# Kernel tuning notes

Measured on AMD Instinct MI355X. Metric: run time of the kernel, lower is better.

Reference implementation:

```python
import jax, jax.numpy as jnp
import numpy as np

B, N, D, S = 128, 1024, 512, 64
ITERS = 3
EPS = 1e-8


def setup_inputs() -> dict:
    key = jax.random.key(0)
    ks = jax.random.split(key, 10)
    inp = {
        "inputs_pe": jax.random.normal(ks[0], (B, N, D), dtype=jnp.float32),
        "inputs": jax.random.normal(ks[1], (B, N, D), dtype=jnp.float32),
        "slots": jax.random.normal(ks[2], (1, S, D), dtype=jnp.float32),
        "W1": jax.random.normal(ks[3], (D, D), dtype=jnp.float32) * 0.02,
        "b1": jnp.zeros((D,), dtype=jnp.float32),
        "W2": jax.random.normal(ks[4], (D, D), dtype=jnp.float32) * 0.02,
        "b2": jnp.zeros((D,), dtype=jnp.float32),
        "W3": jax.random.normal(ks[5], (D, D), dtype=jnp.float32) * 0.02,
        "b3": jnp.zeros((D,), dtype=jnp.float32),
    }
    return inp


def reference(inputs_pe, inputs, slots, W1, b1, W2, b2, W3, b3):
    b = inputs_pe.shape[0]
    scale = D ** (-0.5)
    # to_k: Linear -> ReLU -> Linear -> ReLU -> Linear (torch Linear: x @ W.T + b)
    h = jax.nn.relu(jnp.einsum('bnd,ed->bne', inputs_pe, W1) + b1)
    h = jax.nn.relu(jnp.einsum('bnd,ed->bne', h, W2) + b2)
    k = jnp.einsum('bnd,ed->bne', h, W3) + b3  # [b, n, d]

    q = jnp.broadcast_to(slots, (b, S, D))  # slots never updated in the loop
    for _ in range(ITERS):
        dots = jnp.einsum('bid,bjd->bij', q, k) * scale  # [b, S, n]
        s_j = dots.sum(axis=2, keepdims=True)            # sum over keys j -> [b, S, 1]
        s_all = dots.sum(axis=(1, 2), keepdims=True)     # total per batch -> [b, 1, 1]
        dots = dots / s_j * s_all
        attn = jax.nn.sigmoid(dots)
        attn2 = attn / (attn.sum(axis=-1, keepdims=True) + EPS)
        updates = jnp.einsum('bjd,bij->bid', inputs, attn2)  # [b, S, d]
    return updates, attn
```

## Files before the change

kernel.cpp:

```cpp
#include <hip/hip_runtime.h>
#include <stdint.h>

#define Bb 128
#define Nn 1024
#define Dd 512
#define Ss 64

constexpr float kScale = 0.044194173824159216f;
constexpr float kEps = 1e-8f;

typedef __bf16 bf16x8 __attribute__((ext_vector_type(8)));
typedef float f32x4 __attribute__((ext_vector_type(4)));
typedef float f32x16 __attribute__((ext_vector_type(16)));

__device__ inline unsigned short f2bf_rne(float x) {
  unsigned u = __builtin_bit_cast(unsigned, x);
  u += 0x7FFFu + ((u >> 16) & 1u);
  return (unsigned short)(u >> 16);
}
__device__ inline float bf2f(unsigned short h) {
  unsigned u = ((unsigned)h) << 16;
  return __builtin_bit_cast(float, u);
}

__device__ inline void gl_lds16(const void* g, void* l) {
  typedef unsigned int u32;
  auto gp = (u32 __attribute__((address_space(1)))*)(unsigned long long)(uintptr_t)g;
  auto lp = (u32 __attribute__((address_space(3)))*)(unsigned int)(uintptr_t)l;
  __builtin_amdgcn_global_load_lds(gp, lp, 16, 0, 0);
}

__global__ void cast_split(const float* __restrict__ in,
                           unsigned short* __restrict__ hi,
                           unsigned short* __restrict__ lo,
                           int n4) {
  int i = blockIdx.x * blockDim.x + threadIdx.x;
  const int stride = gridDim.x * blockDim.x;
  for (; i < n4; i += stride) {
    const float4 v = ((const float4*)in)[i];
    ushort4 h, lw;
    h.x = f2bf_rne(v.x); lw.x = f2bf_rne(v.x - bf2f(h.x));
    h.y = f2bf_rne(v.y); lw.y = f2bf_rne(v.y - bf2f(h.y));
    h.z = f2bf_rne(v.z); lw.z = f2bf_rne(v.z - bf2f(h.z));
    h.w = f2bf_rne(v.w); lw.w = f2bf_rne(v.w - bf2f(h.w));
    ((ushort4*)hi)[i] = h;
    ((ushort4*)lo)[i] = lw;
  }
}

template <int ACT>
__global__ __launch_bounds__(512, 1) void gemm_full(
    const unsigned short* __restrict__ Ah, const unsigned short* __restrict__ Al,
    const unsigned short* __restrict__ Wh, const unsigned short* __restrict__ Wl,
    const float* __restrict__ bias,
    unsigned short* __restrict__ Ch, unsigned short* __restrict__ Cl) {
  constexpr int K = 512, BK = 16;
  constexpr int NT = K / BK;
  constexpr int BUF = 20480;
  extern __shared__ unsigned short lds[];
  const int t = threadIdx.x, l = t & 63, w = t >> 6;
  const int wr = w >> 2, wc = w & 3;
  const long rowA0 = (long)blockIdx.x * 128;

  const int p = w >> 2, q = w & 3;
  const unsigned short* srcA = (p ? Al : Ah) + (rowA0 + q * 32 + (l >> 1)) * K + (l & 1) * 8;
  const int s0 = w * 2, s1 = w * 2 + 1;
  const unsigned short* srcWh0 = Wh + (long)(s0 * 32 + (l >> 1)) * K + (l & 1) * 8;
  const unsigned short* srcWh1 = Wh + (long)(s1 * 32 + (l >> 1)) * K + (l & 1) * 8;
  const unsigned short* srcWl0 = Wl + (long)(s0 * 32 + (l >> 1)) * K + (l & 1) * 8;
  const unsigned short* srcWl1 = Wl + (long)(s1 * 32 + (l >> 1)) * K + (l & 1) * 8;
  const int dA = p * 2048 + q * 512;

#define GSTAGE(bufi, koff)                                    \
  {                                                           \
    unsigned short* bq = lds + (bufi)*BUF;                    \
    gl_lds16(srcA + (koff), bq + dA);                         \
    gl_lds16(srcWh0 + (koff), bq + 4096 + s0 * 512);          \
    gl_lds16(srcWh1 + (koff), bq + 4096 + s1 * 512);          \
    gl_lds16(srcWl0 + (koff), bq + 12288 + s0 * 512);         \
    gl_lds16(srcWl1 + (koff), bq + 12288 + s1 * 512);         \
  }

  const int fra = (l & 31) * 16 + (l >> 5) * 8;

  f32x16 acc[2][4] = {};

  GSTAGE(0, 0);
  GSTAGE(1, BK);

  for (int tt = 0; tt < NT; ++tt) {
    if (tt < NT - 1) {
      asm volatile("s_waitcnt vmcnt(5)" ::: "memory");
    } else {
      asm volatile("s_waitcnt vmcnt(0)" ::: "memory");
    }
    __builtin_amdgcn_s_barrier();
    __builtin_amdgcn_sched_barrier(0);
    if (tt < NT - 2) GSTAGE((tt + 2) % 3, (tt + 2) * BK);

    const unsigned short* bufc = lds + (tt % 3) * BUF;
    bf16x8 fah[2], fal[2], fbh[4], fbl[4];
#pragma unroll
    for (int m = 0; m < 2; m++) {
      fah[m] = *(const bf16x8*)(bufc + wr * 1024 + m * 512 + fra);
      fal[m] = *(const bf16x8*)(bufc + 2048 + wr * 1024 + m * 512 + fra);
    }
#pragma unroll
    for (int n = 0; n < 4; n++) {
      fbh[n] = *(const bf16x8*)(bufc + 4096 + wc * 2048 + n * 512 + fra);
      fbl[n] = *(const bf16x8*)(bufc + 12288 + wc * 2048 + n * 512 + fra);
    }
    __builtin_amdgcn_s_setprio(1);
#pragma unroll
    for (int m = 0; m < 2; m++)
#pragma unroll
      for (int n = 0; n < 4; n++) {
        acc[m][n] = __builtin_amdgcn_mfma_f32_32x32x16_bf16(fah[m], fbh[n], acc[m][n], 0, 0, 0);
        acc[m][n] = __builtin_amdgcn_mfma_f32_32x32x16_bf16(fal[m], fbh[n], acc[m][n], 0, 0, 0);
        acc[m][n] = __builtin_amdgcn_mfma_f32_32x32x16_bf16(fah[m], fbl[n], acc[m][n], 0, 0, 0);
      }
    __builtin_amdgcn_s_setprio(0);
    __builtin_amdgcn_sched_barrier(0);
  }
#undef GSTAGE

#pragma unroll
  for (int m = 0; m < 2; m++)
#pragma unroll
    for (int n = 0; n < 4; n++) {
      const int col = wc * 128 + n * 32 + (l & 31);
      const float bv = bias[col];
#pragma unroll
      for (int r = 0; r < 16; r++) {
        const long row = rowA0 + wr * 64 + m * 32 + (r & 3) + 8 * (r >> 2) + 4 * (l >> 5);
        float x = acc[m][n][r] + bv;
        if (ACT) x = fmaxf(x, 0.0f);
        const unsigned short h = f2bf_rne(x);
        const long idx = row * 512 + col;
        Ch[idx] = h;
        Cl[idx] = f2bf_rne(x - bf2f(h));
      }
    }
}

__global__ __launch_bounds__(256) void gemm_dots_split(
    const unsigned short* __restrict__ Qh, const unsigned short* __restrict__ Ql,
    const unsigned short* __restrict__ Kh, const unsigned short* __restrict__ Kl,
    float* __restrict__ dots) {
  constexpr int K = 512, BM = 64, BN = 128, BK = 32;
  __shared__ __align__(16) unsigned short lah[BM * BK];
  __shared__ __align__(16) unsigned short lal[BM * BK];
  __shared__ __align__(16) unsigned short lbh[BN * BK];
  __shared__ __align__(16) unsigned short lbl[BN * BK];
  const int t = threadIdx.x, l = t & 63, w = t >> 6;
  const int b = blockIdx.x >> 3, bc = blockIdx.x & 7;
  const unsigned short* kh = Kh + (long)b * Nn * Dd;
  const unsigned short* kl = Kl + (long)b * Nn * Dd;
  f32x4 acc[4][2] = {};

  for (int k0 = 0; k0 < K; k0 += BK) {
    {
      const int c = t;
      const int ga = (c >> 2) * K + k0 + (c & 3) * 8;
      const int lo = (w * 64) * 8;
      gl_lds16(Qh + ga, lah + lo);
      gl_lds16(Ql + ga, lal + lo);
    }
#pragma unroll
    for (int qq = 0; qq < 2; qq++) {
      const int c = qq * 256 + t;
      const long gb = (long)(bc * BN + (c >> 2)) * K + k0 + (c & 3) * 8;
      const int lo = (qq * 256 + w * 64) * 8;
      gl_lds16(kh + gb, lbh + lo);
      gl_lds16(kl + gb, lbl + lo);
    }
    __syncthreads();
    bf16x8 ah[4], al[4], bh[2], bl[2];
#pragma unroll
    for (int m = 0; m < 4; m++) {
      const int off = (m * 16 + (l & 15)) * BK + (l >> 4) * 8;
      ah[m] = *(const bf16x8*)(lah + off);
      al[m] = *(const bf16x8*)(lal + off);
    }
#pragma unroll
    for (int n = 0; n < 2; n++) {
      const int off = (w * 32 + n * 16 + (l & 15)) * BK + (l >> 4) * 8;
      bh[n] = *(const bf16x8*)(lbh + off);
      bl[n] = *(const bf16x8*)(lbl + off);
    }
#pragma unroll
    for (int m = 0; m < 4; m++)
#pragma unroll
      for (int n = 0; n < 2; n++) {
        acc[m][n] = __builtin_amdgcn_mfma_f32_16x16x32_bf16(ah[m], bh[n], acc[m][n], 0, 0, 0);
        acc[m][n] = __builtin_amdgcn_mfma_f32_16x16x32_bf16(al[m], bh[n], acc[m][n], 0, 0, 0);
        acc[m][n] = __builtin_amdgcn_mfma_f32_16x16x32_bf16(ah[m], bl[n], acc[m][n], 0, 0, 0);
      }
    __syncthreads();
  }
  float* dp = dots + (long)b * Ss * Nn;
#pragma unroll
  for (int m = 0; m < 4; m++) {
    const int row = m * 16 + (l >> 4) * 4;
#pragma unroll
    for (int n = 0; n < 2; n++) {
      const int col = bc * BN + w * 32 + n * 16 + (l & 15);
#pragma unroll
      for (int r = 0; r < 4; r++) dp[(long)(row + r) * Nn + col] = acc[m][n][r] * kScale;
    }
  }
}

__global__ __launch_bounds__(256) void reduce_k(
    const float* __restrict__ dots, float* __restrict__ s_j, float* __restrict__ s_all) {
  const int b = blockIdx.x;
  const int t = threadIdx.x;
  const float* dp = dots + (long)b * Ss * Nn;
  const int i = t >> 2, qq = t & 3;
  float s = 0.f;
  const float* rp = dp + i * Nn + qq * 256;
  for (int j = 0; j < 256; j++) s += rp[j];
  __shared__ float part[256];
  __shared__ float rowsum[64];
  part[t] = s;
  __syncthreads();
  if (t < 64) {
    const float v = part[t * 4] + part[t * 4 + 1] + part[t * 4 + 2] + part[t * 4 + 3];
    rowsum[t] = v;
    s_j[b * 64 + t] = v;
  }
  __syncthreads();
  if (t == 0) {
    float tot = 0.f;
    for (int k = 0; k < 64; k++) tot += rowsum[k];
    s_all[b] = tot;
  }
}

__global__ __launch_bounds__(256) void attn_k(
    const float* __restrict__ dots, const float* __restrict__ s_j,
    const float* __restrict__ s_all, float* __restrict__ attn_out,
    float* __restrict__ inv_r) {
  const int bi = blockIdx.x;
  const int b = bi >> 6;
  const int t = threadIdx.x;
  const float ratio = s_all[b] / s_j[bi];
  const float* dp = dots + (long)bi * Nn;
  float* ap = attn_out + (long)bi * Nn;
  float s = 0.f;
#pragma unroll
  for (int qq = 0; qq < 4; qq++) {
    const int j = qq * 256 + t;
    const float x = dp[j] * ratio;
    const float a = 1.f / (1.f + expf(-x));
    ap[j] = a;
    s += a;
  }
  __shared__ float red[256];
  red[t] = s;
  __syncthreads();
  for (int off = 128; off > 0; off >>= 1) {
    if (t < off) red[t] += red[t + off];
    __syncthreads();
  }
  if (t == 0) inv_r[bi] = 1.f / (red[0] + kEps);
}

__global__ __launch_bounds__(256, 1) void updates_k2(
    const float* __restrict__ attn, const float* __restrict__ inputs,
    const float* __restrict__ inv_r, float* __restrict__ out0) {
  constexpr int NT2 = 32;
  constexpr int BUF_F = 10240;
  extern __shared__ float ldsf[];
  const int t = threadIdx.x, lam = t & 63, w = t >> 6;
  const int b = blockIdx.x >> 1, dt = blockIdx.x & 1;
  const int ig = t >> 5, dg = t & 31;
  const float* inb = inputs + (size_t)b * (Nn * Dd) + dt * 256;
  const float* attsrc = attn + (size_t)b * (Ss * Nn) + (size_t)(t >> 2) * Nn + (t & 3) * 8;
  float acc[8][8] = {};
  float4 ga0, ga1, gb0, gb1;

#define UISSUE(bufi, tile, G0, G1)                                        \
  {                                                                       \
    const int j0_ = (tile)*32;                                            \
    G0 = *(const float4*)(attsrc + j0_);                                  \
    G1 = *(const float4*)(attsrc + j0_ + 4);                              \
    float* db_ = ldsf + (bufi)*BUF_F;                                     \
    _Pragma("unroll") for (int i_ = 0; i_ < 8; i_++) {                    \
      const int row_ = i_ * 4 + w;                                        \
      gl_lds16(inb + (size_t)(j0_ + row_) * Dd + lam * 4, db_ + row_ * 256); \
    }                                                                     \
  }

#define UWRITE(bufi, G0, G1)                                              \
  {                                                                       \
    float* ab_ = ldsf + (bufi)*BUF_F + 8192;                              \
    const int col_ = t >> 2;                                              \
    const int r0_ = (t & 3) * 8;                                          \
    ab_[(r0_ + 0) * 64 + col_] = G0.x;                                    \
    ab_[(r0_ + 1) * 64 + col_] = G0.y;                                    \
    ab_[(r0_ + 2) * 64 + col_] = G0.z;                                    \
    ab_[(r0_ + 3) * 64 + col_] = G0.w;                                    \
    ab_[(r0_ + 4) * 64 + col_] = G1.x;                                    \
    ab_[(r0_ + 5) * 64 + col_] = G1.y;                                    \
    ab_[(r0_ + 6) * 64 + col_] = G1.z;                                    \
    ab_[(r0_ + 7) * 64 + col_] = G1.w;                                    \
  }

#define UCOMP(bufi)                                                       \
  {                                                                       \
    const float* db_ = ldsf + (bufi)*BUF_F;                               \
    const float* ab_ = db_ + 8192;                                        \
    _Pragma("unroll 4") for (int jj = 0; jj < 32; jj++) {                 \
      float av[8], vv[8];                                                 \
      *(float4*)&av[0] = *(const float4*)(ab_ + jj * 64 + ig * 8);        \
      *(float4*)&av[4] = *(const float4*)(ab_ + jj * 64 + ig * 8 + 4);    \
      *(float4*)&vv[0] = *(const float4*)(db_ + jj * 256 + dg * 8);       \
      *(float4*)&vv[4] = *(const float4*)(db_ + jj * 256 + dg * 8 + 4);   \
      _Pragma("unroll") for (int m_ = 0; m_ < 8; m_++)                    \
          _Pragma("unroll") for (int n_ = 0; n_ < 8; n_++)                \
              acc[m_][n_] = __builtin_fmaf(av[m_], vv[n_], acc[m_][n_]);  \
    }                                                                     \
  }

  UISSUE(0, 0, ga0, ga1);
  UISSUE(1, 1, gb0, gb1);
  UWRITE(0, ga0, ga1);

  for (int tt = 0; tt < NT2; tt += 2) {
    asm volatile("s_waitcnt vmcnt(10)" ::: "memory");
    UWRITE((tt + 1) % 3, gb0, gb1);
    asm volatile("s_waitcnt lgkmcnt(0)" ::: "memory");
    __builtin_amdgcn_s_barrier();
    __builtin_amdgcn_sched_barrier(0);
    if (tt < NT2 - 2) UISSUE((tt + 2) % 3, tt + 2, ga0, ga1);
    UCOMP(tt % 3);
    if (tt + 1 < NT2 - 1) {
      asm volatile("s_waitcnt vmcnt(10)" ::: "memory");
    } else {
      asm volatile("s_waitcnt vmcnt(0)" ::: "memory");
    }
    if (tt + 1 < NT2 - 1) UWRITE((tt + 2) % 3, ga0, ga1);
    asm volatile("s_waitcnt lgkmcnt(0)" ::: "memory");
    __builtin_amdgcn_s_barrier();
    __builtin_amdgcn_sched_barrier(0);
    if (tt + 1 < NT2 - 2) UISSUE((tt + 3) % 3, tt + 3, gb0, gb1);
    UCOMP((tt + 1) % 3);
  }
#undef UISSUE
#undef UWRITE
#undef UCOMP

#pragma unroll
  for (int m = 0; m < 8; m++) {
    const int i = ig * 8 + m;
    const float ir = inv_r[b * 64 + i];
    float4 o0, o1;
    o0.x = acc[m][0] * ir; o0.y = acc[m][1] * ir; o0.z = acc[m][2] * ir; o0.w = acc[m][3] * ir;
    o1.x = acc[m][4] * ir; o1.y = acc[m][5] * ir; o1.z = acc[m][6] * ir; o1.w = acc[m][7] * ir;
    float* op = out0 + (size_t)(b * 64 + i) * Dd + dt * 256 + dg * 8;
    *(float4*)op = o0;
    *(float4*)(op + 4) = o1;
  }
}

extern "C" void kernel_launch(void* const* d_in, const int* in_sizes, int n_in,
                              void* d_out, int out_size, void* d_ws, size_t ws_size,
                              hipStream_t stream) {
  (void)in_sizes; (void)n_in; (void)out_size; (void)ws_size;
  const float* inputs_pe = (const float*)d_in[0];
  const float* inputs = (const float*)d_in[1];
  const float* slots = (const float*)d_in[2];
  const float* W1 = (const float*)d_in[3];
  const float* b1 = (const float*)d_in[4];
  const float* W2 = (const float*)d_in[5];
  const float* b2 = (const float*)d_in[6];
  const float* W3 = (const float*)d_in[7];
  const float* b3 = (const float*)d_in[8];

  char* ws = (char*)d_ws;
  size_t off = 0;
  auto alloc = [&](size_t bytes) -> void* {
    void* p = ws + off;
    off += (bytes + 255) & ~(size_t)255;
    return p;
  };
  const size_t actB = (size_t)Bb * Nn * Dd * 2;
  unsigned short* Ahi = (unsigned short*)alloc(actB);
  unsigned short* Alo = (unsigned short*)alloc(actB);
  unsigned short* Bhi = (unsigned short*)alloc(actB);
  unsigned short* Blo = (unsigned short*)alloc(actB);
  unsigned short* w1h = (unsigned short*)alloc(Dd * Dd * 2);
  unsigned short* w1l = (unsigned short*)alloc(Dd * Dd * 2);
  unsigned short* w2h = (unsigned short*)alloc(Dd * Dd * 2);
  unsigned short* w2l = (unsigned short*)alloc(Dd * Dd * 2);
  unsigned short* w3h = (unsigned short*)alloc(Dd * Dd * 2);
  unsigned short* w3l = (unsigned short*)alloc(Dd * Dd * 2);
  unsigned short* sh = (unsigned short*)alloc(Ss * Dd * 2);
  unsigned short* sl = (unsigned short*)alloc(Ss * Dd * 2);
  float* dotsb = (float*)alloc((size_t)Bb * Ss * Nn * 4);
  float* s_j = (float*)alloc(Bb * Ss * 4);
  float* s_all = (float*)alloc(Bb * 4);
  float* inv_r = (float*)alloc(Bb * Ss * 4);

  float* out_updates = (float*)d_out;
  float* out_attn = out_updates + (size_t)Bb * Ss * Dd;

  const int kLds = 3 * 40 * 1024;
  hipFuncSetAttribute(reinterpret_cast<const void*>(gemm_full<1>),
                      hipFuncAttributeMaxDynamicSharedMemorySize, kLds);
  hipFuncSetAttribute(reinterpret_cast<const void*>(gemm_full<0>),
                      hipFuncAttributeMaxDynamicSharedMemorySize, kLds);
  hipFuncSetAttribute(reinterpret_cast<const void*>(updates_k2),
                      hipFuncAttributeMaxDynamicSharedMemorySize, kLds);

  cast_split<<<4096, 256, 0, stream>>>(inputs_pe, Ahi, Alo, Bb * Nn * Dd / 4);
  cast_split<<<256, 256, 0, stream>>>(W1, w1h, w1l, Dd * Dd / 4);
  cast_split<<<256, 256, 0, stream>>>(W2, w2h, w2l, Dd * Dd / 4);
  cast_split<<<256, 256, 0, stream>>>(W3, w3h, w3l, Dd * Dd / 4);
  cast_split<<<32, 256, 0, stream>>>(slots, sh, sl, Ss * Dd / 4);

  gemm_full<1><<<1024, 512, kLds, stream>>>(Ahi, Alo, w1h, w1l, b1, Bhi, Blo);
  gemm_full<1><<<1024, 512, kLds, stream>>>(Bhi, Blo, w2h, w2l, b2, Ahi, Alo);
  gemm_full<0><<<1024, 512, kLds, stream>>>(Ahi, Alo, w3h, w3l, b3, Bhi, Blo);

  gemm_dots_split<<<Bb * 8, 256, 0, stream>>>(sh, sl, Bhi, Blo, dotsb);
  reduce_k<<<Bb, 256, 0, stream>>>(dotsb, s_j, s_all);
  attn_k<<<Bb * Ss, 256, 0, stream>>>(dotsb, s_j, s_all, out_attn, inv_r);
  updates_k2<<<Bb * 2, 256, kLds, stream>>>(out_attn, inputs, inv_r, out_updates);
}
```

Measured before the change: 1.166 ms.

## Rewrite MLP GEMMs with 256x256 tiles and hi/lo split K-stream

The three MLP GEMMs now use 256x256 output tiles per block instead of 128x512. The three bf16 split products (hh, lh, hl) are handled as one K-stream of 48 steps: segment 0 is Ah·Wh, 1 is Al·Wh, 2 is Ah·Wl. The kernel also switches to 16x16x32 MFMA with a 4-stage LDS ring, XOR-swizzled LDS layout, and an XCD-aware block remap. The aim is better operand reuse per loaded byte and fewer LDS bank conflicts, in exchange for more accumulator registers and a deeper pipeline that needs 128KB of LDS.

After: 1.321 ms. 13.3% more time.

```diff
diff --git a/kernel.cpp b/kernel.cpp
--- a/kernel.cpp
+++ b/kernel.cpp
@@ -11,7 +11,6 @@
 
 typedef __bf16 bf16x8 __attribute__((ext_vector_type(8)));
 typedef float f32x4 __attribute__((ext_vector_type(4)));
-typedef float f32x16 __attribute__((ext_vector_type(16)));
 
 __device__ inline unsigned short f2bf_rne(float x) {
   unsigned u = __builtin_bit_cast(unsigned, x);
@@ -49,98 +48,98 @@
 }
 
 template <int ACT>
-__global__ __launch_bounds__(512, 1) void gemm_full(
+__global__ __launch_bounds__(512, 1) void gemm_split3(
     const unsigned short* __restrict__ Ah, const unsigned short* __restrict__ Al,
     const unsigned short* __restrict__ Wh, const unsigned short* __restrict__ Wl,
     const float* __restrict__ bias,
     unsigned short* __restrict__ Ch, unsigned short* __restrict__ Cl) {
-  constexpr int K = 512, BK = 16;
-  constexpr int NT = K / BK;
-  constexpr int BUF = 20480;
+  constexpr int NT3 = 48;
   extern __shared__ unsigned short lds[];
   const int t = threadIdx.x, l = t & 63, w = t >> 6;
+  const int x = l & 15;
   const int wr = w >> 2, wc = w & 3;
-  const long rowA0 = (long)blockIdx.x * 128;
-
-  const int p = w >> 2, q = w & 3;
-  const unsigned short* srcA = (p ? Al : Ah) + (rowA0 + q * 32 + (l >> 1)) * K + (l & 1) * 8;
-  const int s0 = w * 2, s1 = w * 2 + 1;
-  const unsigned short* srcWh0 = Wh + (long)(s0 * 32 + (l >> 1)) * K + (l & 1) * 8;
-  const unsigned short* srcWh1 = Wh + (long)(s1 * 32 + (l >> 1)) * K + (l & 1) * 8;
-  const unsigned short* srcWl0 = Wl + (long)(s0 * 32 + (l >> 1)) * K + (l & 1) * 8;
-  const unsigned short* srcWl1 = Wl + (long)(s1 * 32 + (l >> 1)) * K + (l & 1) * 8;
-  const int dA = p * 2048 + q * 512;
-
-#define GSTAGE(bufi, koff)                                    \
-  {                                                           \
-    unsigned short* bq = lds + (bufi)*BUF;                    \
-    gl_lds16(srcA + (koff), bq + dA);                         \
-    gl_lds16(srcWh0 + (koff), bq + 4096 + s0 * 512);          \
-    gl_lds16(srcWh1 + (koff), bq + 4096 + s1 * 512);          \
-    gl_lds16(srcWl0 + (koff), bq + 12288 + s0 * 512);         \
-    gl_lds16(srcWl1 + (koff), bq + 12288 + s1 * 512);         \
-  }
-
-  const int fra = (l & 31) * 16 + (l >> 5) * 8;
-
-  f32x16 acc[2][4] = {};
-
-  GSTAGE(0, 0);
-  GSTAGE(1, BK);
-
-  for (int tt = 0; tt < NT; ++tt) {
-    if (tt < NT - 1) {
-      asm volatile("s_waitcnt vmcnt(5)" ::: "memory");
+
+  const int wg = (blockIdx.x & 7) * 128 + (blockIdx.x >> 3);
+  const long rowA0 = (long)(wg >> 1) * 256;
+  const int colB0 = (wg & 1) * 256;
+  const unsigned short* Ahb = Ah + rowA0 * 512;
+  const unsigned short* Alb = Al + rowA0 * 512;
+  const unsigned short* Whb = Wh + (long)colB0 * 512;
+  const unsigned short* Wlb = Wl + (long)colB0 * 512;
+
+  const int g0 = (t & 3) ^ (((t >> 2) >> 1) & 3);
+  const int offT0 = (t >> 2) * 512 + g0 * 8;
+  const int offT1 = offT0 + 65536;
+  const int wdst = w * 512;
+
+  auto stage = [&](int kt) {
+    const int seg = kt >> 4;
+    const int k0 = (kt & 15) * 32;
+    const unsigned short* As = (seg == 1) ? Alb : Ahb;
+    const unsigned short* Bs = (seg == 2) ? Wlb : Whb;
+    unsigned short* lb = lds + (kt & 3) * 16384;
+    gl_lds16(As + offT0 + k0, lb + wdst);
+    gl_lds16(As + offT1 + k0, lb + 4096 + wdst);
+    gl_lds16(Bs + offT0 + k0, lb + 8192 + wdst);
+    gl_lds16(Bs + offT1 + k0, lb + 12288 + wdst);
+  };
+
+  const int p16 = ((l >> 4) ^ ((x >> 1) & 3)) * 16;
+  const int abase = (wr * 128 + x) * 64 + p16;
+  const int bbase = 16384 + (wc * 64 + x) * 64 + p16;
+
+  f32x4 acc[8][4] = {};
+
+  stage(0);
+  stage(1);
+  stage(2);
+
+  for (int kt = 0; kt < NT3; ++kt) {
+    if (kt < NT3 - 2) {
+      asm volatile("s_waitcnt vmcnt(8)" ::: "memory");
+    } else if (kt == NT3 - 2) {
+      asm volatile("s_waitcnt vmcnt(4)" ::: "memory");
     } else {
       asm volatile("s_waitcnt vmcnt(0)" ::: "memory");
     }
     __builtin_amdgcn_s_barrier();
     __builtin_amdgcn_sched_barrier(0);
-    if (tt < NT - 2) GSTAGE((tt + 2) % 3, (tt + 2) * BK);
-
-    const unsigned short* bufc = lds + (tt % 3) * BUF;
-    bf16x8 fah[2], fal[2], fbh[4], fbl[4];
-#pragma unroll
-    for (int m = 0; m < 2; m++) {
-      fah[m] = *(const bf16x8*)(bufc + wr * 1024 + m * 512 + fra);
-      fal[m] = *(const bf16x8*)(bufc + 2048 + wr * 1024 + m * 512 + fra);
-    }
-#pragma unroll
-    for (int n = 0; n < 4; n++) {
-      fbh[n] = *(const bf16x8*)(bufc + 4096 + wc * 2048 + n * 512 + fra);
-      fbl[n] = *(const bf16x8*)(bufc + 12288 + wc * 2048 + n * 512 + fra);
-    }
+    if (kt + 3 < NT3) stage(kt + 3);
+
+    const char* bb = (const char*)lds + (kt & 3) * 32768;
+    bf16x8 fb[4], fa[8];
+#pragma unroll
+    for (int n = 0; n < 4; n++) fb[n] = *(const bf16x8*)(bb + bbase + n * 1024);
+#pragma unroll
+    for (int m = 0; m < 8; m++) fa[m] = *(const bf16x8*)(bb + abase + m * 1024);
     __builtin_amdgcn_s_setprio(1);
 #pragma unroll
-    for (int m = 0; m < 2; m++)
-#pragma unroll
-      for (int n = 0; n < 4; n++) {
-        acc[m][n] = __builtin_amdgcn_mfma_f32_32x32x16_bf16(fah[m], fbh[n], acc[m][n], 0, 0, 0);
-        acc[m][n] = __builtin_amdgcn_mfma_f32_32x32x16_bf16(fal[m], fbh[n], acc[m][n], 0, 0, 0);
-        acc[m][n] = __builtin_amdgcn_mfma_f32_32x32x16_bf16(fah[m], fbl[n], acc[m][n], 0, 0, 0);
-      }
+    for (int m = 0; m < 8; m++)
+#pragma unroll
+      for (int n = 0; n < 4; n++)
+        acc[m][n] = __builtin_amdgcn_mfma_f32_16x16x32_bf16(fa[m], fb[n], acc[m][n], 0, 0, 0);
     __builtin_amdgcn_s_setprio(0);
     __builtin_amdgcn_sched_barrier(0);
   }
-#undef GSTAGE
-
-#pragma unroll
-  for (int m = 0; m < 2; m++)
-#pragma unroll
-    for (int n = 0; n < 4; n++) {
-      const int col = wc * 128 + n * 32 + (l & 31);
-      const float bv = bias[col];
-#pragma unroll
-      for (int r = 0; r < 16; r++) {
-        const long row = rowA0 + wr * 64 + m * 32 + (r & 3) + 8 * (r >> 2) + 4 * (l >> 5);
-        float x = acc[m][n][r] + bv;
-        if (ACT) x = fmaxf(x, 0.0f);
-        const unsigned short h = f2bf_rne(x);
-        const long idx = row * 512 + col;
+
+#pragma unroll
+  for (int n = 0; n < 4; n++) {
+    const int col = colB0 + wc * 64 + n * 16 + x;
+    const float bv = bias[col];
+#pragma unroll
+    for (int m = 0; m < 8; m++) {
+      const long row = rowA0 + wr * 128 + m * 16 + (l >> 4) * 4;
+#pragma unroll
+      for (int r = 0; r < 4; r++) {
+        float xv = acc[m][n][r] + bv;
+        if (ACT) xv = fmaxf(xv, 0.0f);
+        const unsigned short h = f2bf_rne(xv);
+        const long idx = (row + r) * 512 + col;
         Ch[idx] = h;
-        Cl[idx] = f2bf_rne(x - bf2f(h));
+        Cl[idx] = f2bf_rne(xv - bf2f(h));
       }
     }
+  }
 }
 
 __global__ __launch_bounds__(256) void gemm_dots_split(
@@ -406,13 +405,14 @@
   float* out_updates = (float*)d_out;
   float* out_attn = out_updates + (size_t)Bb * Ss * Dd;
 
-  const int kLds = 3 * 40 * 1024;
-  hipFuncSetAttribute(reinterpret_cast<const void*>(gemm_full<1>),
-                      hipFuncAttributeMaxDynamicSharedMemorySize, kLds);
-  hipFuncSetAttribute(reinterpret_cast<const void*>(gemm_full<0>),
-                      hipFuncAttributeMaxDynamicSharedMemorySize, kLds);
+  const int kLdsG = 4 * 32 * 1024;
+  const int kLdsU = 3 * 40 * 1024;
+  hipFuncSetAttribute(reinterpret_cast<const void*>(gemm_split3<1>),
+                      hipFuncAttributeMaxDynamicSharedMemorySize, kLdsG);
+  hipFuncSetAttribute(reinterpret_cast<const void*>(gemm_split3<0>),
+                      hipFuncAttributeMaxDynamicSharedMemorySize, kLdsG);
   hipFuncSetAttribute(reinterpret_cast<const void*>(updates_k2),
-                      hipFuncAttributeMaxDynamicSharedMemorySize, kLds);
+                      hipFuncAttributeMaxDynamicSharedMemorySize, kLdsU);
 
   cast_split<<<4096, 256, 0, stream>>>(inputs_pe, Ahi, Alo, Bb * Nn * Dd / 4);
   cast_split<<<256, 256, 0, stream>>>(W1, w1h, w1l, Dd * Dd / 4);
@@ -420,12 +420,12 @@
   cast_split<<<256, 256, 0, stream>>>(W3, w3h, w3l, Dd * Dd / 4);
   cast_split<<<32, 256, 0, stream>>>(slots, sh, sl, Ss * Dd / 4);
 
-  gemm_full<1><<<1024, 512, kLds, stream>>>(Ahi, Alo, w1h, w1l, b1, Bhi, Blo);
-  gemm_full<1><<<1024, 512, kLds, stream>>>(Bhi, Blo, w2h, w2l, b2, Ahi, Alo);
-  gemm_full<0><<<1024, 512, kLds, stream>>>(Ahi, Alo, w3h, w3l, b3, Bhi, Blo);
+  gemm_split3<1><<<1024, 512, kLdsG, stream>>>(Ahi, Alo, w1h, w1l, b1, Bhi, Blo);
+  gemm_split3<1><<<1024, 512, kLdsG, stream>>>(Bhi, Blo, w2h, w2l, b2, Ahi, Alo);
+  gemm_split3<0><<<1024, 512, kLdsG, stream>>>(Ahi, Alo, w3h, w3l, b3, Bhi, Blo);
 
   gemm_dots_split<<<Bb * 8, 256, 0, stream>>>(sh, sl, Bhi, Blo, dotsb);
   reduce_k<<<Bb, 256, 0, stream>>>(dotsb, s_j, s_all);
   attn_k<<<Bb * Ss, 256, 0, stream>>>(dotsb, s_j, s_all, out_attn, inv_r);
-  updates_k2<<<Bb * 2, 256, kLds, stream>>>(out_attn, inputs, inv_r, out_updates);
-}
+  updates_k2<<<Bb * 2, 256, kLdsU, stream>>>(out_attn, inputs, inv_r, out_updates);
+}
```

## Swizzle GEMM LDS layout and prefetch next A fragments with ping-pong registers

Applied to the files above, without the earlier changes.

Rewrites the MLP GEMM main loop. The LDS layout is XOR-swizzled by row parity to reduce bank conflicts, and the loop is unrolled by two so the next tile's A fragments are read from LDS into alternate registers while the current MFMAs run. It also changes the global-to-LDS staging so each wave issues five loads, and the wait becomes vmcnt(0) instead of vmcnt(5). The full wait may stall on the most recently issued prefetch, which could reduce load/compute overlap. The extra fragment registers also raise register pressure.

Measured after the change: 1.192 ms. +2.3%, slower.

```diff
diff --git a/kernel.cpp b/kernel.cpp
--- a/kernel.cpp
+++ b/kernel.cpp
@@ -49,80 +49,100 @@
 }
 
 template <int ACT>
-__global__ __launch_bounds__(512, 1) void gemm_full(
+__global__ __launch_bounds__(512, 1) void gemm_fused3(
     const unsigned short* __restrict__ Ah, const unsigned short* __restrict__ Al,
     const unsigned short* __restrict__ Wh, const unsigned short* __restrict__ Wl,
     const float* __restrict__ bias,
     unsigned short* __restrict__ Ch, unsigned short* __restrict__ Cl) {
-  constexpr int K = 512, BK = 16;
-  constexpr int NT = K / BK;
-  constexpr int BUF = 20480;
+  constexpr int NT = 32;
+  constexpr int BUFU = 20480;
   extern __shared__ unsigned short lds[];
   const int t = threadIdx.x, l = t & 63, w = t >> 6;
   const int wr = w >> 2, wc = w & 3;
   const long rowA0 = (long)blockIdx.x * 128;
 
-  const int p = w >> 2, q = w & 3;
-  const unsigned short* srcA = (p ? Al : Ah) + (rowA0 + q * 32 + (l >> 1)) * K + (l & 1) * 8;
-  const int s0 = w * 2, s1 = w * 2 + 1;
-  const unsigned short* srcWh0 = Wh + (long)(s0 * 32 + (l >> 1)) * K + (l & 1) * 8;
-  const unsigned short* srcWh1 = Wh + (long)(s1 * 32 + (l >> 1)) * K + (l & 1) * 8;
-  const unsigned short* srcWl0 = Wl + (long)(s0 * 32 + (l >> 1)) * K + (l & 1) * 8;
-  const unsigned short* srcWl1 = Wl + (long)(s1 * 32 + (l >> 1)) * K + (l & 1) * 8;
-  const int dA = p * 2048 + q * 512;
-
-#define GSTAGE(bufi, koff)                                    \
-  {                                                           \
-    unsigned short* bq = lds + (bufi)*BUF;                    \
-    gl_lds16(srcA + (koff), bq + dA);                         \
-    gl_lds16(srcWh0 + (koff), bq + 4096 + s0 * 512);          \
-    gl_lds16(srcWh1 + (koff), bq + 4096 + s1 * 512);          \
-    gl_lds16(srcWl0 + (koff), bq + 12288 + s0 * 512);         \
-    gl_lds16(srcWl1 + (koff), bq + 12288 + s1 * 512);         \
-  }
-
-  const int fra = (l & 31) * 16 + (l >> 5) * 8;
+  const unsigned short* gsrc[5];
+  int gdst[5];
+#pragma unroll
+  for (int j = 0; j < 5; j++) {
+    const int id = w * 5 + j;
+    const int rloc = l >> 1;
+    const unsigned short* base;
+    int r;
+    if (id < 4)       { base = Ah + rowA0 * 512; r = id * 32 + rloc; }
+    else if (id < 8)  { base = Al + rowA0 * 512; r = (id - 4) * 32 + rloc; }
+    else if (id < 24) { base = Wh;               r = (id - 8) * 32 + rloc; }
+    else              { base = Wl;               r = (id - 24) * 32 + rloc; }
+    const int g = (l & 1) ^ (r & 1);
+    gsrc[j] = base + (long)r * 512 + g * 8;
+    gdst[j] = id * 512;
+  }
+
+#define FSTAGE(kt)                                                       \
+  {                                                                      \
+    unsigned short* sb_ = lds + ((kt) % 3) * BUFU;                       \
+    _Pragma("unroll") for (int j = 0; j < 5; j++)                        \
+        gl_lds16(gsrc[j] + (kt) * 16, sb_ + gdst[j]);                    \
+  }
+
+  const int lane31 = l & 31;
+  const int pos8 = (((l >> 5) ^ (l & 1))) * 8;
+  const int arow = (wr * 64 + lane31) * 16 + pos8;
+  const int brow = 4096 + (wc * 128 + lane31) * 16 + pos8;
+
+#define FREADA(kt, AH, AL)                                               \
+  {                                                                      \
+    const unsigned short* sb_ = lds + ((kt) % 3) * BUFU;                 \
+    _Pragma("unroll") for (int m = 0; m < 2; m++) {                      \
+      AH[m] = *(const bf16x8*)(sb_ + arow + m * 512);                    \
+      AL[m] = *(const bf16x8*)(sb_ + 2048 + arow + m * 512);             \
+    }                                                                    \
+  }
+#define FREADB(kt)                                                       \
+  {                                                                      \
+    const unsigned short* sb_ = lds + ((kt) % 3) * BUFU;                 \
+    _Pragma("unroll") for (int n = 0; n < 4; n++) {                      \
+      bh[n] = *(const bf16x8*)(sb_ + brow + n * 512);                    \
+      bl[n] = *(const bf16x8*)(sb_ + 8192 + brow + n * 512);             \
+    }                                                                    \
+  }
+
+#define FBODY(kt, AC, ALC, AN, ALN)                                     \
+  {                                                                     \
+    asm volatile("s_waitcnt vmcnt(0)" ::: "memory");                    \
+    __builtin_amdgcn_s_barrier();                                       \
+    __builtin_amdgcn_sched_barrier(0);                                  \
+    if ((kt) + 2 < NT) FSTAGE((kt) + 2);                                \
+    FREADB(kt);                                                         \
+    if ((kt) + 1 < NT) FREADA((kt) + 1, AN, ALN);                       \
+    __builtin_amdgcn_s_setprio(1);                                      \
+    _Pragma("unroll") for (int m = 0; m < 2; m++)                       \
+        _Pragma("unroll") for (int n = 0; n < 4; n++) {                 \
+      acc[m][n] = __builtin_amdgcn_mfma_f32_32x32x16_bf16(AC[m], bh[n], acc[m][n], 0, 0, 0);  \
+      acc[m][n] = __builtin_amdgcn_mfma_f32_32x32x16_bf16(ALC[m], bh[n], acc[m][n], 0, 0, 0); \
+      acc[m][n] = __builtin_amdgcn_mfma_f32_32x32x16_bf16(AC[m], bl[n], acc[m][n], 0, 0, 0);  \
+    }                                                                   \
+    __builtin_amdgcn_s_setprio(0);                                      \
+    __builtin_amdgcn_sched_barrier(0);                                  \
+  }
 
   f32x16 acc[2][4] = {};
-
-  GSTAGE(0, 0);
-  GSTAGE(1, BK);
-
-  for (int tt = 0; tt < NT; ++tt) {
-    if (tt < NT - 1) {
-      asm volatile("s_waitcnt vmcnt(5)" ::: "memory");
-    } else {
-      asm volatile("s_waitcnt vmcnt(0)" ::: "memory");
-    }
-    __builtin_amdgcn_s_barrier();
-    __builtin_amdgcn_sched_barrier(0);
-    if (tt < NT - 2) GSTAGE((tt + 2) % 3, (tt + 2) * BK);
-
-    const unsigned short* bufc = lds + (tt % 3) * BUF;
-    bf16x8 fah[2], fal[2], fbh[4], fbl[4];
-#pragma unroll
-    for (int m = 0; m < 2; m++) {
-      fah[m] = *(const bf16x8*)(bufc + wr * 1024 + m * 512 + fra);
-      fal[m] = *(const bf16x8*)(bufc + 2048 + wr * 1024 + m * 512 + fra);
-    }
-#pragma unroll
-    for (int n = 0; n < 4; n++) {
-      fbh[n] = *(const bf16x8*)(bufc + 4096 + wc * 2048 + n * 512 + fra);
-      fbl[n] = *(const bf16x8*)(bufc + 12288 + wc * 2048 + n * 512 + fra);
-    }
-    __builtin_amdgcn_s_setprio(1);
-#pragma unroll
-    for (int m = 0; m < 2; m++)
-#pragma unroll
-      for (int n = 0; n < 4; n++) {
-        acc[m][n] = __builtin_amdgcn_mfma_f32_32x32x16_bf16(fah[m], fbh[n], acc[m][n], 0, 0, 0);
-        acc[m][n] = __builtin_amdgcn_mfma_f32_32x32x16_bf16(fal[m], fbh[n], acc[m][n], 0, 0, 0);
-        acc[m][n] = __builtin_amdgcn_mfma_f32_32x32x16_bf16(fah[m], fbl[n], acc[m][n], 0, 0, 0);
-      }
-    __builtin_amdgcn_s_setprio(0);
-    __builtin_amdgcn_sched_barrier(0);
-  }
-#undef GSTAGE
+  bf16x8 ahA[2], alA[2], ahB[2], alB[2], bh[4], bl[4];
+
+  FSTAGE(0);
+  FSTAGE(1);
+  asm volatile("s_waitcnt vmcnt(5)" ::: "memory");
+  __builtin_amdgcn_s_barrier();
+  FREADA(0, ahA, alA);
+
+  for (int kt = 0; kt < NT; kt += 2) {
+    FBODY(kt, ahA, alA, ahB, alB);
+    FBODY(kt + 1, ahB, alB, ahA, alA);
+  }
+#undef FSTAGE
+#undef FREADA
+#undef FREADB
+#undef FBODY
 
 #pragma unroll
   for (int m = 0; m < 2; m++)
@@ -133,12 +153,12 @@
 #pragma unroll
       for (int r = 0; r < 16; r++) {
         const long row = rowA0 + wr * 64 + m * 32 + (r & 3) + 8 * (r >> 2) + 4 * (l >> 5);
-        float x = acc[m][n][r] + bv;
-        if (ACT) x = fmaxf(x, 0.0f);
-        const unsigned short h = f2bf_rne(x);
+        float xv = acc[m][n][r] + bv;
+        if (ACT) xv = fmaxf(xv, 0.0f);
+        const unsigned short h = f2bf_rne(xv);
         const long idx = row * 512 + col;
         Ch[idx] = h;
-        Cl[idx] = f2bf_rne(x - bf2f(h));
+        Cl[idx] = f2bf_rne(xv - bf2f(h));
       }
     }
 }
@@ -406,13 +426,14 @@
   float* out_updates = (float*)d_out;
   float* out_attn = out_updates + (size_t)Bb * Ss * Dd;
 
-  const int kLds = 3 * 40 * 1024;
-  hipFuncSetAttribute(reinterpret_cast<const void*>(gemm_full<1>),
-                      hipFuncAttributeMaxDynamicSharedMemorySize, kLds);
-  hipFuncSetAttribute(reinterpret_cast<const void*>(gemm_full<0>),
-                      hipFuncAttributeMaxDynamicSharedMemorySize, kLds);
+  const int kLdsG = 3 * 40 * 1024;
+  const int kLdsU = 3 * 40 * 1024;
+  hipFuncSetAttribute(reinterpret_cast<const void*>(gemm_fused3<1>),
+                      hipFuncAttributeMaxDynamicSharedMemorySize, kLdsG);
+  hipFuncSetAttribute(reinterpret_cast<const void*>(gemm_fused3<0>),
+                      hipFuncAttributeMaxDynamicSharedMemorySize, kLdsG);
   hipFuncSetAttribute(reinterpret_cast<const void*>(updates_k2),
-                      hipFuncAttributeMaxDynamicSharedMemorySize, kLds);
+                      hipFuncAttributeMaxDynamicSharedMemorySize, kLdsU);
 
   cast_split<<<4096, 256, 0, stream>>>(inputs_pe, Ahi, Alo, Bb * Nn * Dd / 4);
   cast_split<<<256, 256, 0, stream>>>(W1, w1h, w1l, Dd * Dd / 4);
@@ -420,12 +441,12 @@
   cast_split<<<256, 256, 0, stream>>>(W3, w3h, w3l, Dd * Dd / 4);
   cast_split<<<32, 256, 0, stream>>>(slots, sh, sl, Ss * Dd / 4);
 
-  gemm_full<1><<<1024, 512, kLds, stream>>>(Ahi, Alo, w1h, w1l, b1, Bhi, Blo);
-  gemm_full<1><<<1024, 512, kLds, stream>>>(Bhi, Blo, w2h, w2l, b2, Ahi, Alo);
-  gemm_full<0><<<1024, 512, kLds, stream>>>(Ahi, Alo, w3h, w3l, b3, Bhi, Blo);
+  gemm_fused3<1><<<1024, 512, kLdsG, stream>>>(Ahi, Alo, w1h, w1l, b1, Bhi, Blo);
+  gemm_fused3<1><<<1024, 512, kLdsG, stream>>>(Bhi, Blo, w2h, w2l, b2, Ahi, Alo);
+  gemm_fused3<0><<<1024, 512, kLdsG, stream>>>(Ahi, Alo, w3h, w3l, b3, Bhi, Blo);
 
   gemm_dots_split<<<Bb * 8, 256, 0, stream>>>(sh, sl, Bhi, Blo, dotsb);
   reduce_k<<<Bb, 256, 0, stream>>>(dotsb, s_j, s_all);
   attn_k<<<Bb * Ss, 256, 0, stream>>>(dotsb, s_j, s_all, out_attn, inv_r);
-  updates_k2<<<Bb * 2, 256, kLds, stream>>>(out_attn, inputs, inv_r, out_updates);
-}
+  updates_k2<<<Bb * 2, 256, kLdsU, stream>>>(out_attn, inputs, inv_r, out_updates);
+}
```
